# Kernel optimization log

Measured on AMD Instinct MI355X. Metric: run time of the kernel, lower is better.

The kernel has to match this reference:

```python
import jax, jax.numpy as jnp
import numpy as np

B, C, N = 4, 512, 4096
C8 = C // 8


def setup_inputs() -> dict:
    key = jax.random.key(0)
    ks = jax.random.split(key, 7)
    s = 0.02
    return {
        "x": jax.random.normal(ks[0], (B, C, N), dtype=jnp.float32),
        "Wq": jax.random.normal(ks[1], (C8, C), dtype=jnp.float32) * s,
        "bq": jax.random.normal(ks[2], (C8,), dtype=jnp.float32) * s,
        "Wk": jax.random.normal(ks[3], (C8, C), dtype=jnp.float32) * s,
        "bk": jax.random.normal(ks[4], (C8,), dtype=jnp.float32) * s,
        "Wv": jax.random.normal(ks[5], (C, C), dtype=jnp.float32) * s,
        "bv": jax.random.normal(ks[6], (C,), dtype=jnp.float32) * s,
        "gamma": jnp.float32(1.0),
    }


def reference(x, Wq, bq, Wk, bk, Wv, bv, gamma):
    # kernel-size-1 Conv1d == per-position channel linear map
    # x: [B, C, N]
    q = jnp.einsum("bcn,dc->bnd", x, Wq) + bq              # [B, N, C8] (query permuted)
    k = jnp.einsum("bcn,dc->bdn", x, Wk) + bk[None, :, None]  # [B, C8, N]
    v = jnp.einsum("bcn,dc->bdn", x, Wv) + bv[None, :, None]  # [B, C, N]
    qk = jnp.einsum("bnd,bdm->bnm", q, k)                  # [B, Nq, Nk]
    # NOTE: softmax over dim=1 (the QUERY axis), as in the original torch code
    attn = jax.nn.softmax(qk, axis=1)                      # [B, Nq, Nk]
    out_attn = jnp.einsum("bcn,bnm->bcm", v, attn)         # value @ attn, [B, C, N]
    return gamma * out_attn + x
```

## Files before the change

kernel.cpp:

```cpp
#include <hip/hip_runtime.h>
#include <hip/hip_bf16.h>

#define BB 4
#define CC 512
#define NN 4096
#define DD 64

typedef __attribute__((ext_vector_type(8))) short short8;
typedef __attribute__((ext_vector_type(4))) short short4v;
typedef __attribute__((ext_vector_type(4))) float floatx4;

static __device__ __forceinline__ short f2bf(float f) {
  __hip_bfloat16 h = __float2bfloat16(f);
  return *reinterpret_cast<short*>(&h);
}

static __device__ __forceinline__ floatx4 mfma16(short8 a, short8 b, floatx4 c) {
  return __builtin_amdgcn_mfma_f32_16x16x32_bf16(a, b, c, 0, 0, 0);
}

__global__ void wconv_kernel(const float* __restrict__ Wq, const float* __restrict__ Wk,
                             const float* __restrict__ Wv, short* __restrict__ Wb) {
  int i = blockIdx.x * 256 + threadIdx.x;
  int row = i >> 9, c = i & 511;
  float v;
  if (row < 64)        v = Wq[(row << 9) | c];
  else if (row < 128)  v = Wk[((row - 64) << 9) | c];
  else                 v = Wv[((row - 128) << 9) | c];
  Wb[i] = f2bf(v);
}

__global__ __launch_bounds__(512, 4) void qkv_kernel(
    const float* __restrict__ x, const short* __restrict__ Wb,
    const float* __restrict__ bq, const float* __restrict__ bk,
    const float* __restrict__ bv,
    short* __restrict__ qb, short* __restrict__ kb, short* __restrict__ vb) {
  const int b  = blockIdx.x >> 7;
  const int n0 = (blockIdx.x & 127) << 5;
  const int tid = threadIdx.x;
  const int w = tid >> 6, lane = tid & 63;
  const int arow = lane & 15, grp = lane >> 4;

  __shared__ short xs[32][72];

  floatx4 acc[2][5];
  #pragma unroll
  for (int i = 0; i < 2; ++i)
    #pragma unroll
    for (int j = 0; j < 5; ++j) acc[i][j] = (floatx4){0.f, 0.f, 0.f, 0.f};

  const float* xb = x + (size_t)b * CC * NN;
  const int cidx = tid >> 3;
  const int n4   = (tid & 7) << 2;

  for (int c0 = 0; c0 < CC; c0 += 64) {
    floatx4 v4 = *(const floatx4*)(xb + (size_t)(c0 + cidx) * NN + n0 + n4);
    __syncthreads();
    #pragma unroll
    for (int i = 0; i < 4; ++i) xs[n4 + i][cidx] = f2bf(v4[i]);
    __syncthreads();
    #pragma unroll
    for (int ks = 0; ks < 2; ++ks) {
      short8 afr[2];
      #pragma unroll
      for (int ns = 0; ns < 2; ++ns)
        afr[ns] = *(const short8*)&xs[ns * 16 + arow][ks * 32 + grp * 8];
      #pragma unroll
      for (int ds = 0; ds < 5; ++ds) {
        const short* wp = Wb + (size_t)(w * 80 + ds * 16 + arow) * CC + c0 + ks * 32 + grp * 8;
        short8 bfr = *(const short8*)wp;
        #pragma unroll
        for (int ns = 0; ns < 2; ++ns)
          acc[ns][ds] = mfma16(afr[ns], bfr, acc[ns][ds]);
      }
    }
  }

  #pragma unroll
  for (int ds = 0; ds < 5; ++ds) {
    int dout = w * 80 + ds * 16 + arow;
    float bias = (dout < 64) ? bq[dout] : (dout < 128) ? bk[dout - 64] : bv[dout - 128];
    #pragma unroll
    for (int ns = 0; ns < 2; ++ns) {
      int nrow = n0 + ns * 16 + grp * 4;
      floatx4 a = acc[ns][ds];
      if (dout < 64) {
        #pragma unroll
        for (int r = 0; r < 4; ++r)
          qb[((size_t)b * NN + nrow + r) * DD + dout] = f2bf(a[r] + bias);
      } else if (dout < 128) {
        #pragma unroll
        for (int r = 0; r < 4; ++r)
          kb[((size_t)b * NN + nrow + r) * DD + (dout - 64)] = f2bf(a[r] + bias);
      } else {
        short4v pk;
        #pragma unroll
        for (int r = 0; r < 4; ++r) pk[r] = f2bf(a[r] + bias);
        *(short4v*)(vb + ((size_t)b * CC + (dout - 128)) * NN + nrow) = pk;
      }
    }
  }
}

__global__ __launch_bounds__(512, 4) void attn_kernel(
    const short* __restrict__ qb, const short* __restrict__ kb,
    const short* __restrict__ vb, const float* __restrict__ x,
    const float* __restrict__ gamma, float* __restrict__ out) {
  const int bm = blockIdx.x >> 1;
  const int ch = blockIdx.x & 1;
  const int b  = bm >> 6;
  const int m0 = (bm & 63) << 6;
  const int tid = threadIdx.x;
  const int w = tid >> 6, lane = tid & 63;
  const int arow = lane & 15, grp = lane >> 4;
  const int nsub = w & 3;

  __shared__ short pbuf[2][64][72];
  __shared__ float dsum[4][64];

  const short* qB = qb + (size_t)b * NN * DD;
  const short* kB = kb + (size_t)b * NN * DD;
  const short* vB = vb + (size_t)b * CC * NN;

  short8 afr[2][2];
  #pragma unroll
  for (int h = 0; h < 2; ++h) {
    int msub = (w >> 2) + 2 * h;
    const short* kr = kB + (size_t)(m0 + msub * 16 + arow) * DD;
    afr[h][0] = *(const short8*)(kr + grp * 8);
    afr[h][1] = *(const short8*)(kr + 32 + grp * 8);
  }

  floatx4 acc[4][2];
  #pragma unroll
  for (int i = 0; i < 4; ++i)
    #pragma unroll
    for (int j = 0; j < 2; ++j) acc[i][j] = (floatx4){0.f, 0.f, 0.f, 0.f};
  float dl[2][4];
  #pragma unroll
  for (int h = 0; h < 2; ++h)
    #pragma unroll
    for (int r = 0; r < 4; ++r) dl[h][r] = 0.f;

  const int c0w = ch * 256 + w * 32;

  const short* qr0 = qB + (size_t)(nsub * 16 + arow) * DD + grp * 8;
  short8 q0 = *(const short8*)(qr0);
  short8 q1 = *(const short8*)(qr0 + 32);

  int buf = 0;
  for (int nb = 0; nb < NN; nb += 64) {
    #pragma unroll
    for (int h = 0; h < 2; ++h) {
      int msub = (w >> 2) + 2 * h;
      floatx4 s4 = (floatx4){0.f, 0.f, 0.f, 0.f};
      s4 = mfma16(afr[h][0], q0, s4);
      s4 = mfma16(afr[h][1], q1, s4);
      int mloc = msub * 16 + grp * 4;
      #pragma unroll
      for (int r = 0; r < 4; ++r) {
        float p = __expf(s4[r]);
        dl[h][r] += p;
        pbuf[buf][mloc + r][nsub * 16 + arow] = f2bf(p);
      }
    }
    {
      int nbn = (nb + 64) & (NN - 1);
      const short* qr = qB + (size_t)(nbn + nsub * 16 + arow) * DD + grp * 8;
      q0 = *(const short8*)(qr);
      q1 = *(const short8*)(qr + 32);
    }
    short8 vr0[2];
    #pragma unroll
    for (int cs = 0; cs < 2; ++cs)
      vr0[cs] = *(const short8*)(vB + (size_t)(c0w + cs * 16 + arow) * NN + nb + grp * 8);
    __syncthreads();
    short8 pa[4];
    #pragma unroll
    for (int ms = 0; ms < 4; ++ms)
      pa[ms] = *(const short8*)&pbuf[buf][ms * 16 + arow][grp * 8];
    short8 vr1[2];
    #pragma unroll
    for (int cs = 0; cs < 2; ++cs)
      vr1[cs] = *(const short8*)(vB + (size_t)(c0w + cs * 16 + arow) * NN + nb + 32 + grp * 8);
    #pragma unroll
    for (int cs = 0; cs < 2; ++cs)
      #pragma unroll
      for (int ms = 0; ms < 4; ++ms)
        acc[ms][cs] = mfma16(pa[ms], vr0[cs], acc[ms][cs]);
    #pragma unroll
    for (int ms = 0; ms < 4; ++ms)
      pa[ms] = *(const short8*)&pbuf[buf][ms * 16 + arow][32 + grp * 8];
    #pragma unroll
    for (int cs = 0; cs < 2; ++cs)
      #pragma unroll
      for (int ms = 0; ms < 4; ++ms)
        acc[ms][cs] = mfma16(pa[ms], vr1[cs], acc[ms][cs]);
    buf ^= 1;
  }

  #pragma unroll
  for (int off = 1; off < 16; off <<= 1)
    #pragma unroll
    for (int h = 0; h < 2; ++h)
      #pragma unroll
      for (int r = 0; r < 4; ++r)
        dl[h][r] += __shfl_xor(dl[h][r], off);
  if (arow == 0) {
    #pragma unroll
    for (int h = 0; h < 2; ++h) {
      int msub = (w >> 2) + 2 * h;
      #pragma unroll
      for (int r = 0; r < 4; ++r)
        dsum[nsub][msub * 16 + grp * 4 + r] = dl[h][r];
    }
  }
  __syncthreads();

  const float g = *gamma;
  #pragma unroll
  for (int ms = 0; ms < 4; ++ms) {
    int mloc = ms * 16 + grp * 4;
    int mrow = m0 + mloc;
    floatx4 linv;
    #pragma unroll
    for (int r = 0; r < 4; ++r) {
      float l = dsum[0][mloc + r] + dsum[1][mloc + r] + dsum[2][mloc + r] + dsum[3][mloc + r];
      linv[r] = g / l;
    }
    #pragma unroll
    for (int cs = 0; cs < 2; ++cs) {
      int c = c0w + cs * 16 + arow;
      const float* xp = x + ((size_t)b * CC + c) * NN + mrow;
      floatx4 xv = *(const floatx4*)xp;
      floatx4 res;
      #pragma unroll
      for (int r = 0; r < 4; ++r) res[r] = acc[ms][cs][r] * linv[r] + xv[r];
      *(floatx4*)(out + ((size_t)b * CC + c) * NN + mrow) = res;
    }
  }
}

extern "C" void kernel_launch(void* const* d_in, const int* in_sizes, int n_in,
                              void* d_out, int out_size, void* d_ws, size_t ws_size,
                              hipStream_t stream) {
  const float* x     = (const float*)d_in[0];
  const float* Wq    = (const float*)d_in[1];
  const float* bq    = (const float*)d_in[2];
  const float* Wk    = (const float*)d_in[3];
  const float* bk    = (const float*)d_in[4];
  const float* Wv    = (const float*)d_in[5];
  const float* bv    = (const float*)d_in[6];
  const float* gamma = (const float*)d_in[7];
  float* out = (float*)d_out;

  char* ws = (char*)d_ws;
  short* qb = (short*)(ws);
  short* kb = (short*)(ws + (2u << 20));
  short* vb = (short*)(ws + (4u << 20));
  short* Wb = (short*)(ws + (21u << 20));

  hipLaunchKernelGGL(wconv_kernel, dim3(1280), dim3(256), 0, stream, Wq, Wk, Wv, Wb);
  hipLaunchKernelGGL(qkv_kernel, dim3(BB * 128), dim3(512), 0, stream,
                     x, Wb, bq, bk, bv, qb, kb, vb);
  hipLaunchKernelGGL(attn_kernel, dim3(BB * 64 * 2), dim3(512), 0, stream,
                     qb, kb, vb, x, gamma, out);
}
```

Baseline: 314.9 us.

## Retile QKV projection and software-pipeline attention with triple-buffered swizzled P tile

The QKV projection kernel now tiles 128 positions by 128 output channels per block, prefetching the next x chunk into registers while the current one is converted and multiplied. The attention kernel now computes the next score tile before the current P·V step, using a three-slot XOR-swizzled LDS buffer. It also changes the warp split to 32 rows by 64 channels, remaps block ids so each XCD handles one batch/channel-half, and raises wave priority around the MFMA block. These aim to overlap exp/score work with MFMA, cut LDS bank conflicts and improve L2 locality of V, at the cost of more registers and LDS.

```diff
diff --git a/kernel.cpp b/kernel.cpp
--- a/kernel.cpp
+++ b/kernel.cpp
@@ -35,68 +35,87 @@
     const float* __restrict__ bq, const float* __restrict__ bk,
     const float* __restrict__ bv,
     short* __restrict__ qb, short* __restrict__ kb, short* __restrict__ vb) {
-  const int b  = blockIdx.x >> 7;
-  const int n0 = (blockIdx.x & 127) << 5;
+  const int bid = blockIdx.x;
+  const int jt = bid % 5;
+  const int mt = bid / 5;
+  const int b  = mt >> 5;
+  const int n0 = (mt & 31) << 7;
   const int tid = threadIdx.x;
   const int w = tid >> 6, lane = tid & 63;
   const int arow = lane & 15, grp = lane >> 4;
-
-  __shared__ short xs[32][72];
-
-  floatx4 acc[2][5];
-  #pragma unroll
-  for (int i = 0; i < 2; ++i)
-    #pragma unroll
-    for (int j = 0; j < 5; ++j) acc[i][j] = (floatx4){0.f, 0.f, 0.f, 0.f};
+  const int wm = w >> 2, wj = w & 3;
+
+  __shared__ short xs[128][72];
 
   const float* xb = x + (size_t)b * CC * NN;
-  const int cidx = tid >> 3;
-  const int n4   = (tid & 7) << 2;
-
-  for (int c0 = 0; c0 < CC; c0 += 64) {
-    floatx4 v4 = *(const floatx4*)(xb + (size_t)(c0 + cidx) * NN + n0 + n4);
+  const int n4l = (tid & 31) << 2;
+  const int c4  = (tid >> 5) << 2;
+
+  floatx4 ld[4];
+  #pragma unroll
+  for (int i = 0; i < 4; ++i)
+    ld[i] = *(const floatx4*)(xb + (size_t)(c4 + i) * NN + n0 + n4l);
+
+  floatx4 acc[4][2];
+  #pragma unroll
+  for (int i = 0; i < 4; ++i)
+    #pragma unroll
+    for (int j = 0; j < 2; ++j) acc[i][j] = (floatx4){0.f, 0.f, 0.f, 0.f};
+
+  for (int kk = 0; kk < 8; ++kk) {
     __syncthreads();
     #pragma unroll
-    for (int i = 0; i < 4; ++i) xs[n4 + i][cidx] = f2bf(v4[i]);
+    for (int j = 0; j < 4; ++j) {
+      short4v pk;
+      #pragma unroll
+      for (int i = 0; i < 4; ++i) pk[i] = f2bf(ld[i][j]);
+      *(short4v*)&xs[n4l + j][c4] = pk;
+    }
     __syncthreads();
+    if (kk < 7) {
+      #pragma unroll
+      for (int i = 0; i < 4; ++i)
+        ld[i] = *(const floatx4*)(xb + (size_t)((kk + 1) * 64 + c4 + i) * NN + n0 + n4l);
+    }
     #pragma unroll
     for (int ks = 0; ks < 2; ++ks) {
-      short8 afr[2];
-      #pragma unroll
-      for (int ns = 0; ns < 2; ++ns)
-        afr[ns] = *(const short8*)&xs[ns * 16 + arow][ks * 32 + grp * 8];
-      #pragma unroll
-      for (int ds = 0; ds < 5; ++ds) {
-        const short* wp = Wb + (size_t)(w * 80 + ds * 16 + arow) * CC + c0 + ks * 32 + grp * 8;
+      short8 pa[4];
+      #pragma unroll
+      for (int ms = 0; ms < 4; ++ms)
+        pa[ms] = *(const short8*)&xs[wm * 64 + ms * 16 + arow][ks * 32 + grp * 8];
+      #pragma unroll
+      for (int js = 0; js < 2; ++js) {
+        const short* wp = Wb + (size_t)(jt * 128 + wj * 32 + js * 16 + arow) * CC
+                        + kk * 64 + ks * 32 + grp * 8;
         short8 bfr = *(const short8*)wp;
         #pragma unroll
-        for (int ns = 0; ns < 2; ++ns)
-          acc[ns][ds] = mfma16(afr[ns], bfr, acc[ns][ds]);
+        for (int ms = 0; ms < 4; ++ms)
+          acc[ms][js] = mfma16(pa[ms], bfr, acc[ms][js]);
       }
     }
   }
 
   #pragma unroll
-  for (int ds = 0; ds < 5; ++ds) {
-    int dout = w * 80 + ds * 16 + arow;
+  for (int js = 0; js < 2; ++js) {
+    int dout = jt * 128 + wj * 32 + js * 16 + arow;
     float bias = (dout < 64) ? bq[dout] : (dout < 128) ? bk[dout - 64] : bv[dout - 128];
     #pragma unroll
-    for (int ns = 0; ns < 2; ++ns) {
-      int nrow = n0 + ns * 16 + grp * 4;
-      floatx4 a = acc[ns][ds];
+    for (int ms = 0; ms < 4; ++ms) {
+      int n = n0 + wm * 64 + ms * 16 + grp * 4;
+      floatx4 a = acc[ms][js];
       if (dout < 64) {
         #pragma unroll
         for (int r = 0; r < 4; ++r)
-          qb[((size_t)b * NN + nrow + r) * DD + dout] = f2bf(a[r] + bias);
+          qb[((size_t)b * NN + n + r) * DD + dout] = f2bf(a[r] + bias);
       } else if (dout < 128) {
         #pragma unroll
         for (int r = 0; r < 4; ++r)
-          kb[((size_t)b * NN + nrow + r) * DD + (dout - 64)] = f2bf(a[r] + bias);
+          kb[((size_t)b * NN + n + r) * DD + (dout - 64)] = f2bf(a[r] + bias);
       } else {
         short4v pk;
         #pragma unroll
         for (int r = 0; r < 4; ++r) pk[r] = f2bf(a[r] + bias);
-        *(short4v*)(vb + ((size_t)b * CC + (dout - 128)) * NN + nrow) = pk;
+        *(short4v*)(vb + ((size_t)b * CC + (dout - 128)) * NN + n) = pk;
       }
     }
   }
@@ -106,97 +125,125 @@
     const short* __restrict__ qb, const short* __restrict__ kb,
     const short* __restrict__ vb, const float* __restrict__ x,
     const float* __restrict__ gamma, float* __restrict__ out) {
-  const int bm = blockIdx.x >> 1;
-  const int ch = blockIdx.x & 1;
-  const int b  = bm >> 6;
-  const int m0 = (bm & 63) << 6;
+  const int bid = blockIdx.x;
+  const int xcd = bid & 7;
+  const int b = xcd >> 1, ch = xcd & 1;
+  const int m0 = (bid >> 3) << 6;
   const int tid = threadIdx.x;
   const int w = tid >> 6, lane = tid & 63;
   const int arow = lane & 15, grp = lane >> 4;
   const int nsub = w & 3;
-
-  __shared__ short pbuf[2][64][72];
+  const int mh = w >> 2;
+  const int wc = w & 3;
+
+  __shared__ short pbuf[3][64 * 64];
   __shared__ float dsum[4][64];
 
   const short* qB = qb + (size_t)b * NN * DD;
   const short* kB = kb + (size_t)b * NN * DD;
-  const short* vB = vb + (size_t)b * CC * NN;
+  const short* vB = vb + ((size_t)b * CC + ch * 256) * NN;
 
   short8 afr[2][2];
   #pragma unroll
   for (int h = 0; h < 2; ++h) {
-    int msub = (w >> 2) + 2 * h;
-    const short* kr = kB + (size_t)(m0 + msub * 16 + arow) * DD;
+    const short* kr = kB + (size_t)(m0 + mh * 32 + h * 16 + arow) * DD;
     afr[h][0] = *(const short8*)(kr + grp * 8);
     afr[h][1] = *(const short8*)(kr + 32 + grp * 8);
   }
 
-  floatx4 acc[4][2];
-  #pragma unroll
-  for (int i = 0; i < 4; ++i)
-    #pragma unroll
-    for (int j = 0; j < 2; ++j) acc[i][j] = (floatx4){0.f, 0.f, 0.f, 0.f};
+  floatx4 acc[2][4];
+  #pragma unroll
+  for (int i = 0; i < 2; ++i)
+    #pragma unroll
+    for (int j = 0; j < 4; ++j) acc[i][j] = (floatx4){0.f, 0.f, 0.f, 0.f};
   float dl[2][4];
   #pragma unroll
   for (int h = 0; h < 2; ++h)
     #pragma unroll
     for (int r = 0; r < 4; ++r) dl[h][r] = 0.f;
 
-  const int c0w = ch * 256 + w * 32;
-
-  const short* qr0 = qB + (size_t)(nsub * 16 + arow) * DD + grp * 8;
-  short8 q0 = *(const short8*)(qr0);
-  short8 q1 = *(const short8*)(qr0 + 32);
-
-  int buf = 0;
-  for (int nb = 0; nb < NN; nb += 64) {
-    #pragma unroll
-    for (int h = 0; h < 2; ++h) {
-      int msub = (w >> 2) + 2 * h;
-      floatx4 s4 = (floatx4){0.f, 0.f, 0.f, 0.f};
-      s4 = mfma16(afr[h][0], q0, s4);
-      s4 = mfma16(afr[h][1], q1, s4);
-      int mloc = msub * 16 + grp * 4;
-      #pragma unroll
-      for (int r = 0; r < 4; ++r) {
-        float p = __expf(s4[r]);
-        dl[h][r] += p;
-        pbuf[buf][mloc + r][nsub * 16 + arow] = f2bf(p);
+  short8 qa0, qa1;
+  {
+    const short* qr = qB + (size_t)(nsub * 16 + arow) * DD + grp * 8;
+    qa0 = *(const short8*)(qr);
+    qa1 = *(const short8*)(qr + 32);
+  }
+
+  #pragma unroll
+  for (int h = 0; h < 2; ++h) {
+    floatx4 s4 = (floatx4){0.f, 0.f, 0.f, 0.f};
+    s4 = mfma16(afr[h][0], qa0, s4);
+    s4 = mfma16(afr[h][1], qa1, s4);
+    int mrow = mh * 32 + h * 16 + grp * 4;
+    #pragma unroll
+    for (int r = 0; r < 4; ++r) {
+      float p = __expf(s4[r]);
+      dl[h][r] += p;
+      int row = mrow + r;
+      pbuf[0][row * 64 + ((nsub * 16 + arow) ^ ((row & 7) << 3))] = f2bf(p);
+    }
+  }
+  {
+    const short* qr = qB + (size_t)(64 + nsub * 16 + arow) * DD + grp * 8;
+    qa0 = *(const short8*)(qr);
+    qa1 = *(const short8*)(qr + 32);
+  }
+
+  int cur = 0;
+  for (int i = 0; i < 64; ++i) {
+    const int nb = i << 6;
+    int nxt = cur + 1; if (nxt == 3) nxt = 0;
+    short8 vv0[4];
+    #pragma unroll
+    for (int cs = 0; cs < 4; ++cs)
+      vv0[cs] = *(const short8*)(vB + (size_t)(wc * 64 + cs * 16 + arow) * NN + nb + grp * 8);
+    if (i < 63) {
+      #pragma unroll
+      for (int h = 0; h < 2; ++h) {
+        floatx4 s4 = (floatx4){0.f, 0.f, 0.f, 0.f};
+        s4 = mfma16(afr[h][0], qa0, s4);
+        s4 = mfma16(afr[h][1], qa1, s4);
+        int mrow = mh * 32 + h * 16 + grp * 4;
+        #pragma unroll
+        for (int r = 0; r < 4; ++r) {
+          float p = __expf(s4[r]);
+          dl[h][r] += p;
+          int row = mrow + r;
+          pbuf[nxt][row * 64 + ((nsub * 16 + arow) ^ ((row & 7) << 3))] = f2bf(p);
+        }
       }
     }
-    {
-      int nbn = (nb + 64) & (NN - 1);
-      const short* qr = qB + (size_t)(nbn + nsub * 16 + arow) * DD + grp * 8;
-      q0 = *(const short8*)(qr);
-      q1 = *(const short8*)(qr + 32);
-    }
-    short8 vr0[2];
-    #pragma unroll
-    for (int cs = 0; cs < 2; ++cs)
-      vr0[cs] = *(const short8*)(vB + (size_t)(c0w + cs * 16 + arow) * NN + nb + grp * 8);
+    if (i < 62) {
+      const short* qr = qB + (size_t)(nb + 128 + nsub * 16 + arow) * DD + grp * 8;
+      qa0 = *(const short8*)(qr);
+      qa1 = *(const short8*)(qr + 32);
+    }
     __syncthreads();
-    short8 pa[4];
-    #pragma unroll
-    for (int ms = 0; ms < 4; ++ms)
-      pa[ms] = *(const short8*)&pbuf[buf][ms * 16 + arow][grp * 8];
-    short8 vr1[2];
-    #pragma unroll
-    for (int cs = 0; cs < 2; ++cs)
-      vr1[cs] = *(const short8*)(vB + (size_t)(c0w + cs * 16 + arow) * NN + nb + 32 + grp * 8);
-    #pragma unroll
-    for (int cs = 0; cs < 2; ++cs)
-      #pragma unroll
-      for (int ms = 0; ms < 4; ++ms)
-        acc[ms][cs] = mfma16(pa[ms], vr0[cs], acc[ms][cs]);
-    #pragma unroll
-    for (int ms = 0; ms < 4; ++ms)
-      pa[ms] = *(const short8*)&pbuf[buf][ms * 16 + arow][32 + grp * 8];
-    #pragma unroll
-    for (int cs = 0; cs < 2; ++cs)
-      #pragma unroll
-      for (int ms = 0; ms < 4; ++ms)
-        acc[ms][cs] = mfma16(pa[ms], vr1[cs], acc[ms][cs]);
-    buf ^= 1;
+    short8 pa[2][2];
+    #pragma unroll
+    for (int ms = 0; ms < 2; ++ms) {
+      int row = mh * 32 + ms * 16 + arow;
+      #pragma unroll
+      for (int ks = 0; ks < 2; ++ks)
+        pa[ms][ks] = *(const short8*)&pbuf[cur][row * 64 + ((ks * 32 + grp * 8) ^ ((row & 7) << 3))];
+    }
+    short8 vv1[4];
+    #pragma unroll
+    for (int cs = 0; cs < 4; ++cs)
+      vv1[cs] = *(const short8*)(vB + (size_t)(wc * 64 + cs * 16 + arow) * NN + nb + 32 + grp * 8);
+    __builtin_amdgcn_s_setprio(1);
+    #pragma unroll
+    for (int cs = 0; cs < 4; ++cs)
+      #pragma unroll
+      for (int ms = 0; ms < 2; ++ms)
+        acc[ms][cs] = mfma16(pa[ms][0], vv0[cs], acc[ms][cs]);
+    #pragma unroll
+    for (int cs = 0; cs < 4; ++cs)
+      #pragma unroll
+      for (int ms = 0; ms < 2; ++ms)
+        acc[ms][cs] = mfma16(pa[ms][1], vv1[cs], acc[ms][cs]);
+    __builtin_amdgcn_s_setprio(0);
+    cur = nxt;
   }
 
   #pragma unroll
@@ -208,35 +255,32 @@
         dl[h][r] += __shfl_xor(dl[h][r], off);
   if (arow == 0) {
     #pragma unroll
-    for (int h = 0; h < 2; ++h) {
-      int msub = (w >> 2) + 2 * h;
+    for (int h = 0; h < 2; ++h)
       #pragma unroll
       for (int r = 0; r < 4; ++r)
-        dsum[nsub][msub * 16 + grp * 4 + r] = dl[h][r];
-    }
+        dsum[nsub][mh * 32 + h * 16 + grp * 4 + r] = dl[h][r];
   }
   __syncthreads();
 
   const float g = *gamma;
   #pragma unroll
-  for (int ms = 0; ms < 4; ++ms) {
-    int mloc = ms * 16 + grp * 4;
-    int mrow = m0 + mloc;
+  for (int ms = 0; ms < 2; ++ms) {
+    int ml = mh * 32 + ms * 16 + grp * 4;
     floatx4 linv;
     #pragma unroll
     for (int r = 0; r < 4; ++r) {
-      float l = dsum[0][mloc + r] + dsum[1][mloc + r] + dsum[2][mloc + r] + dsum[3][mloc + r];
+      float l = dsum[0][ml + r] + dsum[1][ml + r] + dsum[2][ml + r] + dsum[3][ml + r];
       linv[r] = g / l;
     }
     #pragma unroll
-    for (int cs = 0; cs < 2; ++cs) {
-      int c = c0w + cs * 16 + arow;
-      const float* xp = x + ((size_t)b * CC + c) * NN + mrow;
+    for (int cs = 0; cs < 4; ++cs) {
+      int c = ch * 256 + wc * 64 + cs * 16 + arow;
+      const float* xp = x + ((size_t)b * CC + c) * NN + m0 + ml;
       floatx4 xv = *(const floatx4*)xp;
       floatx4 res;
       #pragma unroll
       for (int r = 0; r < 4; ++r) res[r] = acc[ms][cs][r] * linv[r] + xv[r];
-      *(floatx4*)(out + ((size_t)b * CC + c) * NN + mrow) = res;
+      *(floatx4*)(out + ((size_t)b * CC + c) * NN + m0 + ml) = res;
     }
   }
 }
@@ -261,8 +305,8 @@
   short* Wb = (short*)(ws + (21u << 20));
 
   hipLaunchKernelGGL(wconv_kernel, dim3(1280), dim3(256), 0, stream, Wq, Wk, Wv, Wb);
-  hipLaunchKernelGGL(qkv_kernel, dim3(BB * 128), dim3(512), 0, stream,
+  hipLaunchKernelGGL(qkv_kernel, dim3(640), dim3(512), 0, stream,
                      x, Wb, bq, bk, bv, qb, kb, vb);
-  hipLaunchKernelGGL(attn_kernel, dim3(BB * 64 * 2), dim3(512), 0, stream,
+  hipLaunchKernelGGL(attn_kernel, dim3(512), dim3(512), 0, stream,
                      qb, kb, vb, x, gamma, out);
 }
```

Measured after the change: 565.8 us. 79.7% more time.
